# Kernel optimization log

Hardware: AMD Instinct MI355X
Metric: run time of the kernel (lower is better)

Reference implementation:

```python
import jax, jax.numpy as jnp
import numpy as np

S, N, CM, CZ, H, D = 512, 768, 64, 128, 8, 32
EPS = 1e-5


def _layer_norm(x, w, b):
    mu = jnp.mean(x, axis=-1, keepdims=True)
    xc = x - mu
    var = jnp.mean(xc * xc, axis=-1, keepdims=True)
    return xc * jax.lax.rsqrt(var + EPS) * w + b


def setup_inputs() -> dict:
    key = jax.random.key(0)
    ks = jax.random.split(key, 6)
    scale_m = 1.0 / np.sqrt(CM)
    scale_z = 1.0 / np.sqrt(CZ)
    scale_o = 1.0 / np.sqrt(H * D)
    return {
        "m": jax.random.normal(ks[0], (1, S, N, CM), jnp.float32),
        "z": jax.random.normal(ks[1], (1, N, N, CZ), jnp.float32),
        "norm_m_w": jnp.ones((CM,), jnp.float32),
        "norm_m_b": jnp.zeros((CM,), jnp.float32),
        "norm_z_w": jnp.ones((CZ,), jnp.float32),
        "norm_z_b": jnp.zeros((CZ,), jnp.float32),
        "wm": jax.random.normal(ks[2], (CM, H * D), jnp.float32) * scale_m,
        "wg": jax.random.normal(ks[3], (CM, H * D), jnp.float32) * scale_m,
        "wz": jax.random.normal(ks[4], (CZ, H), jnp.float32) * scale_z,
        "wo": jax.random.normal(ks[5], (H * D, CM), jnp.float32) * scale_o,
    }


def reference(m, z, norm_m_w, norm_m_b, norm_z_w, norm_z_b, wm, wg, wz, wo):
    m0 = m[0]  # [S, N, CM]
    z0 = z[0]  # [N, N, CZ]
    mn = _layer_norm(m0, norm_m_w, norm_m_b)
    zn = _layer_norm(z0, norm_z_w, norm_z_b)
    # b[p,q,h]; original code softmaxes over the LAST axis of b'[h,p,q] (axis q)
    # but contracts as o[s,q] = sum_p w[p,q] v[s,p] (transpose_a matmul),
    # so softmax is over axis q = axis 1 of [p,q,h].
    b = jnp.einsum('pqc,ch->pqh', zn, wz)
    w = jax.nn.softmax(b, axis=1)  # normalized over q for each p (faithful to source)
    v = jnp.einsum('spc,ck->spk', mn, wm).reshape(S, N, H, D)
    g = jax.nn.sigmoid(jnp.einsum('spc,ck->spk', mn, wg)).reshape(S, N, H, D)
    o = jnp.einsum('pqh,sphd->sqhd', w, v) * g  # weighted average then gate
    out = jnp.einsum('sqhd,hdc->sqc', o, wo.reshape(H, D, CM))
    return out[None]  # [1, S, N, CM]
```

## Files before the change

### kernel.cpp

```cpp
#include <hip/hip_runtime.h>
#include <hip/hip_bf16.h>
#include <stdint.h>

#define S_DIM 512
#define N_DIM 768
#define CMd   64
#define CZd   128
#define Hd    8
#define Dd    32
#define HDd   256

typedef float          f32x4  __attribute__((ext_vector_type(4)));
typedef __bf16         bf16x8 __attribute__((ext_vector_type(8)));
typedef unsigned int   u32x4  __attribute__((ext_vector_type(4)));
typedef unsigned int   u32x2  __attribute__((ext_vector_type(2)));
typedef unsigned short u16x8  __attribute__((ext_vector_type(8)));

__device__ __forceinline__ unsigned short f2bf(float f) {
  __bf16 h = (__bf16)f;
  return __builtin_bit_cast(unsigned short, h);
}
__device__ __forceinline__ float bf2f(unsigned short u) {
  unsigned int x = ((unsigned int)u) << 16;
  return __builtin_bit_cast(float, x);
}
__device__ __forceinline__ float sigmoidf_(float x) {
  return 1.f / (1.f + __expf(-x));
}

typedef __attribute__((address_space(1))) const void cg_void;
typedef __attribute__((address_space(3))) void lds_void;
__device__ __forceinline__ void async16(const unsigned short* g, unsigned short* l) {
  __builtin_amdgcn_global_load_lds((cg_void*)g, (lds_void*)l, 16, 0, 0);
}

__global__ __launch_bounds__(256) void k0_prep(const float* __restrict__ wm,
                                               const float* __restrict__ wg,
                                               const float* __restrict__ wo,
                                               unsigned short* __restrict__ WBT,
                                               unsigned short* __restrict__ woT) {
  int t = blockIdx.x * 256 + threadIdx.x;
  if (t < 512 * 64) {
    int j = t >> 6, c = t & 63;
    float v = (j < 256) ? wm[c * 256 + j] : wg[c * 256 + (j - 256)];
    WBT[t] = f2bf(v);
  }
  if (t < 64 * 256) {
    int c = t >> 8, k = t & 255;
    woT[t] = f2bf(wo[k * 64 + c]);
  }
}

__global__ __launch_bounds__(256) void k1_zln_b(const float* __restrict__ z,
                                                const float* __restrict__ nzw,
                                                const float* __restrict__ nzb,
                                                const float* __restrict__ wz,
                                                float* __restrict__ b_e) {
  __shared__ float wzT[8][128];
  int t = threadIdx.x;
  for (int i = t; i < 1024; i += 256) {
    int h = i >> 7, c = i & 127;
    wzT[h][c] = wz[c * 8 + h];
  }
  __syncthreads();

  int lane = t & 63, w = t >> 6;
  int sub = lane & 7;
  int rloc = lane >> 3;
  int p = blockIdx.y;
  int q = blockIdx.x * 32 + w * 8 + rloc;

  const float* zr = z + ((size_t)p * N_DIM + q) * CZd + sub * 16;
  f32x4 v[4];
#pragma unroll
  for (int j = 0; j < 4; j++) v[j] = *(const f32x4*)(zr + 4 * j);

  float s1 = 0.f, s2 = 0.f;
#pragma unroll
  for (int j = 0; j < 4; j++)
#pragma unroll
    for (int e = 0; e < 4; e++) { float x = v[j][e]; s1 += x; s2 += x * x; }
  s1 += __shfl_xor(s1, 1); s2 += __shfl_xor(s2, 1);
  s1 += __shfl_xor(s1, 2); s2 += __shfl_xor(s2, 2);
  s1 += __shfl_xor(s1, 4); s2 += __shfl_xor(s2, 4);
  float mean = s1 * (1.f / 128.f);
  float var  = s2 * (1.f / 128.f) - mean * mean;
  float rstd = rsqrtf(var + 1e-5f);

  const float* wp = nzw + sub * 16;
  const float* bp = nzb + sub * 16;
  float zn[16];
#pragma unroll
  for (int j = 0; j < 4; j++) {
    f32x4 wv = *(const f32x4*)(wp + 4 * j);
    f32x4 bv = *(const f32x4*)(bp + 4 * j);
#pragma unroll
    for (int e = 0; e < 4; e++)
      zn[j * 4 + e] = (v[j][e] - mean) * rstd * wv[e] + bv[e];
  }

  float accb[8];
#pragma unroll
  for (int h = 0; h < 8; h++) {
    const f32x4* wr = (const f32x4*)&wzT[h][sub * 16];
    float a = 0.f;
#pragma unroll
    for (int j = 0; j < 4; j++) {
      f32x4 ww = wr[j];
#pragma unroll
      for (int e = 0; e < 4; e++) a += zn[j * 4 + e] * ww[e];
    }
    accb[h] = a;
  }
#pragma unroll
  for (int mask = 1; mask <= 4; mask <<= 1)
#pragma unroll
    for (int h = 0; h < 8; h++) accb[h] += __shfl_xor(accb[h], mask);

  float outv = accb[0];
#pragma unroll
  for (int h = 1; h < 8; h++) outv = (sub == h) ? accb[h] : outv;
  b_e[((size_t)p * 8 + sub) * 768 + q] = outv;
}

__global__ __launch_bounds__(256) void k1b_softmax(float* __restrict__ b_e,
                                                   float* __restrict__ invs) {
  int row = blockIdx.x;
  int t = threadIdx.x;
  float* base = b_e + (size_t)row * 768;
  float x0 = base[t], x1 = base[t + 256], x2 = base[t + 512];
  __shared__ float red[256];
  red[t] = fmaxf(x0, fmaxf(x1, x2));
  __syncthreads();
  for (int o = 128; o > 0; o >>= 1) {
    if (t < o) red[t] = fmaxf(red[t], red[t + o]);
    __syncthreads();
  }
  float M = red[0];
  __syncthreads();
  float e0 = __expf(x0 - M), e1 = __expf(x1 - M), e2 = __expf(x2 - M);
  base[t] = e0; base[t + 256] = e1; base[t + 512] = e2;
  red[t] = e0 + e1 + e2;
  __syncthreads();
  for (int o = 128; o > 0; o >>= 1) {
    if (t < o) red[t] += red[t + o];
    __syncthreads();
  }
  if (t == 0) invs[row] = 1.0f / red[0];
}

__global__ __launch_bounds__(256) void k1b2_transpose(const float* __restrict__ b_e,
                                                      const float* __restrict__ invs,
                                                      unsigned short* __restrict__ Aw) {
  int t = threadIdx.x;
  int q0 = blockIdx.x * 64, p0 = blockIdx.y * 64, h = blockIdx.z;
  __shared__ unsigned short T[64][65];
  int i = t >> 2, ch = t & 3;
  size_t rowid = (size_t)(p0 + i) * 8 + h;
  const float* src = b_e + rowid * 768 + q0 + ch * 16;
  float inv = invs[rowid];
#pragma unroll
  for (int jj = 0; jj < 16; jj += 4) {
    f32x4 v = *(const f32x4*)(src + jj);
#pragma unroll
    for (int e = 0; e < 4; e++) T[i][ch * 16 + jj + e] = f2bf(v[e] * inv);
  }
  __syncthreads();
  int j = i;
  unsigned short outv[16];
#pragma unroll
  for (int ii = 0; ii < 16; ii++) outv[ii] = T[ch * 16 + ii][j];
  int rx = (j & 7) << 3;
  unsigned short* dstrow = Aw + ((size_t)h * 768 + q0 + j) * 768 + p0;
  *(u32x4*)(dstrow + ((ch * 16) ^ rx))     = *(u32x4*)(outv);
  *(u32x4*)(dstrow + ((ch * 16 + 8) ^ rx)) = *(u32x4*)(outv + 8);
}

__global__ __launch_bounds__(256) void k2_mln_vg(const float* __restrict__ mp,
                                                 const float* __restrict__ nmw,
                                                 const float* __restrict__ nmb,
                                                 const unsigned short* __restrict__ WBT,
                                                 unsigned short* __restrict__ VT,
                                                 unsigned short* __restrict__ G) {
  __shared__ unsigned short WBs[512 * 64];
  __shared__ unsigned short As[64 * 64];
  int t = threadIdx.x;
  int p0 = blockIdx.x * 64, s = blockIdx.y;

#pragma unroll
  for (int it = 0; it < 16; it++) {
    int cid = t + it * 256;
    int row = cid >> 3, ch = cid & 7;
    u32x4 v = *(const u32x4*)(WBT + row * 64 + ch * 8);
    *(u32x4*)(WBs + row * 64 + ((ch * 8) ^ ((row & 7) << 3))) = v;
  }

  {
    int row = t >> 2, qt = t & 3;
    const float* mr = mp + ((size_t)s * N_DIM + p0 + row) * CMd + qt * 16;
    f32x4 v[4];
#pragma unroll
    for (int j = 0; j < 4; j++) v[j] = *(const f32x4*)(mr + 4 * j);
    float s1 = 0.f, s2 = 0.f;
#pragma unroll
    for (int j = 0; j < 4; j++)
#pragma unroll
      for (int e = 0; e < 4; e++) { float x = v[j][e]; s1 += x; s2 += x * x; }
    s1 += __shfl_xor(s1, 1); s2 += __shfl_xor(s2, 1);
    s1 += __shfl_xor(s1, 2); s2 += __shfl_xor(s2, 2);
    float mean = s1 * (1.f / 64.f);
    float var  = s2 * (1.f / 64.f) - mean * mean;
    float rstd = rsqrtf(var + 1e-5f);
    unsigned short o[16];
#pragma unroll
    for (int j = 0; j < 4; j++) {
      f32x4 wv = *(const f32x4*)(nmw + qt * 16 + 4 * j);
      f32x4 bv = *(const f32x4*)(nmb + qt * 16 + 4 * j);
#pragma unroll
      for (int e = 0; e < 4; e++)
        o[j * 4 + e] = f2bf((v[j][e] - mean) * rstd * wv[e] + bv[e]);
    }
    int k0 = qt * 16;
    *(u32x4*)(As + row * 64 + ((k0) ^ ((row & 7) << 3)))     = *(u32x4*)(o);
    *(u32x4*)(As + row * 64 + ((k0 + 8) ^ ((row & 7) << 3))) = *(u32x4*)(o + 8);
  }
  __syncthreads();

  int lane = t & 63, w = t >> 6;
  int n0 = w * 128;
  int lr = lane & 15, lk8 = (lane >> 4) * 8;
  f32x4 zero = {0.f, 0.f, 0.f, 0.f};
  f32x4 acc[4][8];
#pragma unroll
  for (int i = 0; i < 4; i++)
#pragma unroll
    for (int j = 0; j < 8; j++) acc[i][j] = zero;

#pragma unroll
  for (int kk = 0; kk < 2; kk++) {
    bf16x8 bfr[8];
#pragma unroll
    for (int nt = 0; nt < 8; nt++) {
      int r = n0 + nt * 16 + lr;
      bfr[nt] = *(const bf16x8*)(WBs + r * 64 + ((kk * 32 + lk8) ^ ((r & 7) << 3)));
    }
#pragma unroll
    for (int mt = 0; mt < 4; mt++) {
      int ar = mt * 16 + lr;
      bf16x8 a = *(const bf16x8*)(As + ar * 64 + ((kk * 32 + lk8) ^ ((ar & 7) << 3)));
#pragma unroll
      for (int nt = 0; nt < 8; nt++)
        acc[mt][nt] = __builtin_amdgcn_mfma_f32_16x16x32_bf16(a, bfr[nt], acc[mt][nt], 0, 0, 0);
    }
  }

#pragma unroll
  for (int mt = 0; mt < 4; mt++)
#pragma unroll
    for (int nt = 0; nt < 8; nt++) {
      int j = n0 + nt * 16 + lr;
      int ploc = mt * 16 + (lane >> 4) * 4;
      if (j < 256) {
        int h = j >> 5, d = j & 31;
        unsigned short pk[4];
#pragma unroll
        for (int r = 0; r < 4; r++) pk[r] = f2bf(acc[mt][nt][r]);
        int pswz = ((((ploc >> 3) ^ (lr & 7)) << 3) | (ploc & 7));
        *(u32x2*)(VT + ((size_t)h * 16384 + s * 32 + d) * 768 + p0 + pswz) = *(u32x2*)pk;
      } else {
        int jj = j - 256;
#pragma unroll
        for (int r = 0; r < 4; r++)
          G[((size_t)s * 768 + p0 + ploc + r) * 256 + jj] = f2bf(sigmoidf_(acc[mt][nt][r]));
      }
    }
}

__global__ __launch_bounds__(256, 3) void k34_fused(const unsigned short* __restrict__ Aw,
                                                    const unsigned short* __restrict__ VT,
                                                    const unsigned short* __restrict__ G,
                                                    const unsigned short* __restrict__ woT,
                                                    float* __restrict__ out) {
  __shared__ unsigned short Asl[64 * 64];
  __shared__ unsigned short Bsl[128 * 64];
  __shared__ unsigned short SLAB[4 * 64 * 40];

  int t = threadIdx.x;
  int flat = blockIdx.x;
  int g = (flat & 7) * 192 + (flat >> 3);
  int q_t = g >> 7, n_t = g & 127;
  int q0 = q_t * 64, n0 = n_t * 128;

  int lane = t & 63, w = t >> 6;
  int lr = lane & 15, lg = lane >> 4;
  int s_w = n_t * 4 + w;

  const size_t aOff = (size_t)(q0 + w * 16 + (lane >> 3)) * 768 + (lane & 7) * 8;
  const size_t bOff = (size_t)(n0 + w * 32 + (lane >> 3)) * 768 + (lane & 7) * 8;
  unsigned short* slab = SLAB + w * 2560;

  f32x4 zero = {0.f, 0.f, 0.f, 0.f};
  f32x4 oh[4][2];
  f32x4 oc[4][4];
#pragma unroll
  for (int i = 0; i < 4; i++) {
#pragma unroll
    for (int j = 0; j < 2; j++) oh[i][j] = zero;
#pragma unroll
    for (int j = 0; j < 4; j++) oc[i][j] = zero;
  }

#pragma unroll 1
  for (int h = 0; h < 8; h++) {
    const unsigned short* Ah = Aw + (size_t)h * 589824;
    const unsigned short* Bh = VT + (size_t)h * 12582912;

#pragma unroll 1
    for (int kt = 0; kt < 12; kt++) {
      int ko = kt * 64;
#pragma unroll
      for (int i = 0; i < 2; i++)
        async16(Ah + aOff + (size_t)i * 8 * 768 + ko, Asl + w * 1024 + i * 512);
#pragma unroll
      for (int i = 0; i < 4; i++)
        async16(Bh + bOff + (size_t)i * 8 * 768 + ko, Bsl + w * 2048 + i * 512);
      asm volatile("s_waitcnt vmcnt(0)" ::: "memory");
      __builtin_amdgcn_sched_barrier(0);
      __syncthreads();
#pragma unroll
      for (int kk = 0; kk < 2; kk++) {
        int kc = kk * 32 + lg * 8;
        bf16x8 afr[4], bfr[2];
#pragma unroll
        for (int mq = 0; mq < 4; mq++) {
          int ar = mq * 16 + lr;
          afr[mq] = *(const bf16x8*)(Asl + ar * 64 + (kc ^ ((ar & 7) << 3)));
        }
#pragma unroll
        for (int j = 0; j < 2; j++) {
          int br = w * 32 + j * 16 + lr;
          bfr[j] = *(const bf16x8*)(Bsl + br * 64 + (kc ^ ((br & 7) << 3)));
        }
#pragma unroll
        for (int mq = 0; mq < 4; mq++)
#pragma unroll
          for (int j = 0; j < 2; j++)
            oh[mq][j] = __builtin_amdgcn_mfma_f32_16x16x32_bf16(afr[mq], bfr[j], oh[mq][j], 0, 0, 0);
      }
      __syncthreads();
    }

    asm volatile("s_waitcnt lgkmcnt(0)" ::: "memory");
    __builtin_amdgcn_sched_barrier(0);

#pragma unroll
    for (int mq = 0; mq < 4; mq++)
#pragma unroll
      for (int j = 0; j < 2; j++) {
        int d = j * 16 + lr;
        const unsigned short* gp =
            G + ((size_t)s_w * 768 + q0 + mq * 16 + lg * 4) * 256 + h * 32 + d;
#pragma unroll
        for (int r = 0; r < 4; r++) {
          float gv = bf2f(gp[(size_t)r * 256]);
          int ql = mq * 16 + lg * 4 + r;
          slab[ql * 40 + d] = f2bf(oh[mq][j][r] * gv);
          oh[mq][j][r] = 0.f;
        }
      }
    asm volatile("s_waitcnt lgkmcnt(0)" ::: "memory");
    __builtin_amdgcn_sched_barrier(0);

    bf16x8 pa[4], wb[4];
#pragma unroll
    for (int mq = 0; mq < 4; mq++)
      pa[mq] = *(const bf16x8*)(slab + (mq * 16 + lr) * 40 + lg * 8);
#pragma unroll
    for (int nc = 0; nc < 4; nc++)
      wb[nc] = *(const bf16x8*)(woT + (size_t)(nc * 16 + lr) * 256 + h * 32 + lg * 8);
#pragma unroll
    for (int mq = 0; mq < 4; mq++)
#pragma unroll
      for (int nc = 0; nc < 4; nc++)
        oc[mq][nc] = __builtin_amdgcn_mfma_f32_16x16x32_bf16(pa[mq], wb[nc], oc[mq][nc], 0, 0, 0);
  }

#pragma unroll
  for (int mq = 0; mq < 4; mq++)
#pragma unroll
    for (int nc = 0; nc < 4; nc++) {
      float* dst = out + ((size_t)s_w * 768 + q0 + mq * 16 + lg * 4) * 64 + nc * 16 + lr;
#pragma unroll
      for (int r = 0; r < 4; r++) dst[(size_t)r * 64] = oc[mq][nc][r];
    }
}

extern "C" void kernel_launch(void* const* d_in, const int* in_sizes, int n_in,
                              void* d_out, int out_size, void* d_ws, size_t ws_size,
                              hipStream_t stream) {
  const float* m   = (const float*)d_in[0];
  const float* z   = (const float*)d_in[1];
  const float* nmw = (const float*)d_in[2];
  const float* nmb = (const float*)d_in[3];
  const float* nzw = (const float*)d_in[4];
  const float* nzb = (const float*)d_in[5];
  const float* wm  = (const float*)d_in[6];
  const float* wg  = (const float*)d_in[7];
  const float* wz  = (const float*)d_in[8];
  const float* wo  = (const float*)d_in[9];
  float* out = (float*)d_out;

  char* ws = (char*)d_ws;
  size_t off = 0;
  auto alloc = [&](size_t bytes) -> void* {
    void* p = ws + off;
    off += (bytes + 1023) & ~(size_t)1023;
    return p;
  };
  float*          b_e  = (float*)alloc((size_t)768 * 8 * 768 * 4);
  float*          invs = (float*)alloc((size_t)768 * 8 * 4);
  unsigned short* Awt  = (unsigned short*)alloc((size_t)8 * 768 * 768 * 2);
  unsigned short* WBT  = (unsigned short*)alloc((size_t)512 * 64 * 2);
  unsigned short* woT  = (unsigned short*)alloc((size_t)64 * 256 * 2);
  unsigned short* VT   = (unsigned short*)alloc((size_t)8 * 16384 * 768 * 2);
  unsigned short* G    = (unsigned short*)alloc((size_t)512 * 768 * 256 * 2);
  if (ws_size < off) return;

  k0_prep<<<128, 256, 0, stream>>>(wm, wg, wo, WBT, woT);
  k1_zln_b<<<dim3(24, 768), 256, 0, stream>>>(z, nzw, nzb, wz, b_e);
  k1b_softmax<<<6144, 256, 0, stream>>>(b_e, invs);
  k1b2_transpose<<<dim3(12, 12, 8), 256, 0, stream>>>(b_e, invs, Awt);
  k2_mln_vg<<<dim3(12, 512), 256, 0, stream>>>(m, nmw, nmb, WBT, VT, G);
  k34_fused<<<dim3(1536), 256, 0, stream>>>(Awt, VT, G, woT, out);
}
```

Measured before the change: 735.3 us.

## Retile fused attention-output kernel so each block owns one s and 384 q rows

The fused weighted-average and output-projection kernel is retiled. Each 384-thread block now handles a single s index and 384 q rows, with each wave owning 64 q rows. Previously a block covered 64 q rows and four s values. The VT (B) tile shrinks to one s's 32 d-rows and is shared by all six waves, and the large A tile is reused as the per-wave gating slab. This changes the reuse balance: V traffic drops, but each block streams far more of the attention-weight matrix and needs more LDS, which may limit occupancy.

Result: slower. 1.070 ms (+45.6%).

```diff
diff --git a/kernel.cpp b/kernel.cpp
--- a/kernel.cpp
+++ b/kernel.cpp
@@ -276,28 +276,25 @@
     }
 }
 
-__global__ __launch_bounds__(256, 3) void k34_fused(const unsigned short* __restrict__ Aw,
+__global__ __launch_bounds__(384, 3) void k34_fused(const unsigned short* __restrict__ Aw,
                                                     const unsigned short* __restrict__ VT,
                                                     const unsigned short* __restrict__ G,
                                                     const unsigned short* __restrict__ woT,
                                                     float* __restrict__ out) {
-  __shared__ unsigned short Asl[64 * 64];
-  __shared__ unsigned short Bsl[128 * 64];
-  __shared__ unsigned short SLAB[4 * 64 * 40];
+  __shared__ unsigned short Asl[384 * 64];
+  __shared__ unsigned short Bsl[32 * 64];
 
   int t = threadIdx.x;
   int flat = blockIdx.x;
-  int g = (flat & 7) * 192 + (flat >> 3);
-  int q_t = g >> 7, n_t = g & 127;
-  int q0 = q_t * 64, n0 = n_t * 128;
-
-  int lane = t & 63, w = t >> 6;
+  int g2 = (flat & 7) * 128 + (flat >> 3);
+  int s = g2 >> 1, qt = g2 & 1;
+  int q0 = qt * 384;
+
+  int lane = t & 63, w = t / 64;
   int lr = lane & 15, lg = lane >> 4;
-  int s_w = n_t * 4 + w;
-
-  const size_t aOff = (size_t)(q0 + w * 16 + (lane >> 3)) * 768 + (lane & 7) * 8;
-  const size_t bOff = (size_t)(n0 + w * 32 + (lane >> 3)) * 768 + (lane & 7) * 8;
-  unsigned short* slab = SLAB + w * 2560;
+
+  const size_t aOff = (size_t)(q0 + w * 64 + (lane >> 3)) * 768 + (lane & 7) * 8;
+  const size_t bOff = ((size_t)s * 32 + w * 8 + (lane >> 3)) * 768 + (lane & 7) * 8;
 
   f32x4 zero = {0.f, 0.f, 0.f, 0.f};
   f32x4 oh[4][2];
@@ -319,11 +316,9 @@
     for (int kt = 0; kt < 12; kt++) {
       int ko = kt * 64;
 #pragma unroll
-      for (int i = 0; i < 2; i++)
-        async16(Ah + aOff + (size_t)i * 8 * 768 + ko, Asl + w * 1024 + i * 512);
-#pragma unroll
-      for (int i = 0; i < 4; i++)
-        async16(Bh + bOff + (size_t)i * 8 * 768 + ko, Bsl + w * 2048 + i * 512);
+      for (int i = 0; i < 8; i++)
+        async16(Ah + aOff + (size_t)i * 8 * 768 + ko, Asl + w * 4096 + i * 512);
+      if (w < 4) async16(Bh + bOff + ko, Bsl + w * 512);
       asm volatile("s_waitcnt vmcnt(0)" ::: "memory");
       __builtin_amdgcn_sched_barrier(0);
       __syncthreads();
@@ -333,13 +328,13 @@
         bf16x8 afr[4], bfr[2];
 #pragma unroll
         for (int mq = 0; mq < 4; mq++) {
-          int ar = mq * 16 + lr;
-          afr[mq] = *(const bf16x8*)(Asl + ar * 64 + (kc ^ ((ar & 7) << 3)));
+          int row = w * 64 + mq * 16 + lr;
+          afr[mq] = *(const bf16x8*)(Asl + row * 64 + (kc ^ ((row & 7) << 3)));
         }
 #pragma unroll
         for (int j = 0; j < 2; j++) {
-          int br = w * 32 + j * 16 + lr;
-          bfr[j] = *(const bf16x8*)(Bsl + br * 64 + (kc ^ ((br & 7) << 3)));
+          int row = j * 16 + lr;
+          bfr[j] = *(const bf16x8*)(Bsl + row * 64 + (kc ^ ((row & 7) << 3)));
         }
 #pragma unroll
         for (int mq = 0; mq < 4; mq++)
@@ -350,16 +345,14 @@
       __syncthreads();
     }
 
-    asm volatile("s_waitcnt lgkmcnt(0)" ::: "memory");
-    __builtin_amdgcn_sched_barrier(0);
-
+    unsigned short* slab = Asl + w * 4096;
 #pragma unroll
     for (int mq = 0; mq < 4; mq++)
 #pragma unroll
       for (int j = 0; j < 2; j++) {
         int d = j * 16 + lr;
         const unsigned short* gp =
-            G + ((size_t)s_w * 768 + q0 + mq * 16 + lg * 4) * 256 + h * 32 + d;
+            G + ((size_t)s * 768 + q0 + w * 64 + mq * 16 + lg * 4) * 256 + h * 32 + d;
 #pragma unroll
         for (int r = 0; r < 4; r++) {
           float gv = bf2f(gp[(size_t)r * 256]);
@@ -370,11 +363,12 @@
       }
     asm volatile("s_waitcnt lgkmcnt(0)" ::: "memory");
     __builtin_amdgcn_sched_barrier(0);
-
     bf16x8 pa[4], wb[4];
 #pragma unroll
     for (int mq = 0; mq < 4; mq++)
       pa[mq] = *(const bf16x8*)(slab + (mq * 16 + lr) * 40 + lg * 8);
+    asm volatile("s_waitcnt lgkmcnt(0)" ::: "memory");
+    __builtin_amdgcn_sched_barrier(0);
 #pragma unroll
     for (int nc = 0; nc < 4; nc++)
       wb[nc] = *(const bf16x8*)(woT + (size_t)(nc * 16 + lr) * 256 + h * 32 + lg * 8);
@@ -389,7 +383,7 @@
   for (int mq = 0; mq < 4; mq++)
 #pragma unroll
     for (int nc = 0; nc < 4; nc++) {
-      float* dst = out + ((size_t)s_w * 768 + q0 + mq * 16 + lg * 4) * 64 + nc * 16 + lr;
+      float* dst = out + ((size_t)s * 768 + q0 + w * 64 + mq * 16 + lg * 4) * 64 + nc * 16 + lr;
 #pragma unroll
       for (int r = 0; r < 4; r++) dst[(size_t)r * 64] = oc[mq][nc][r];
     }
@@ -431,5 +425,5 @@
   k1b_softmax<<<6144, 256, 0, stream>>>(b_e, invs);
   k1b2_transpose<<<dim3(12, 12, 8), 256, 0, stream>>>(b_e, invs, Awt);
   k2_mln_vg<<<dim3(12, 512), 256, 0, stream>>>(m, nmw, nmb, WBT, VT, G);
-  k34_fused<<<dim3(1536), 256, 0, stream>>>(Awt, VT, G, woT, out);
-}
+  k34_fused<<<dim3(1024), 384, 0, stream>>>(Awt, VT, G, woT, out);
+}
```
